# Kernel optimization log

Hardware: AMD Instinct MI355X
Metric: run time of the kernel (lower is better)

The kernel has to match this reference:

```python
import jax, jax.numpy as jnp
import numpy as np

B, S, D, H = 2, 2048, 768, 12
HD = D // H  # head dim = 64

def setup_inputs() -> dict:
    key = jax.random.key(0)
    ks = jax.random.split(key, 9)
    s = 1.0 / np.sqrt(D)
    return {
        "x": jax.random.normal(ks[0], (B, S, D), dtype=jnp.float32),
        "Wq": jax.random.uniform(ks[1], (D, D), jnp.float32, -s, s),
        "bq": jax.random.uniform(ks[2], (D,), jnp.float32, -s, s),
        "Wk": jax.random.uniform(ks[3], (D, D), jnp.float32, -s, s),
        "bk": jax.random.uniform(ks[4], (D,), jnp.float32, -s, s),
        "Wv": jax.random.uniform(ks[5], (D, D), jnp.float32, -s, s),
        "bv": jax.random.uniform(ks[6], (D,), jnp.float32, -s, s),
        "Wo": jax.random.uniform(ks[7], (D, D), jnp.float32, -s, s),
        "bo": jax.random.uniform(ks[8], (D,), jnp.float32, -s, s),
    }

def reference(x, Wq, bq, Wk, bk, Wv, bv, Wo, bo):
    b, s, _ = x.shape
    # linear projections, split into heads: [b, h, s, hd]
    def proj(W, bias):
        y = x @ W + bias
        return y.reshape(b, s, H, HD).transpose(0, 2, 1, 3)
    q = proj(Wq, bq)
    k = proj(Wk, bk)
    v = proj(Wv, bv)
    scale = 1.0 / np.sqrt(HD).astype(np.float32)
    scores = jnp.einsum('bhqd,bhkd->bhqk', q, k) * scale
    attn = jax.nn.softmax(scores, axis=-1)
    out = jnp.einsum('bhqk,bhkd->bhqd', attn, v)
    out = out.transpose(0, 2, 1, 3).reshape(b, s, D)
    return out @ Wo + bo
```

## Files before the change

### kernel.cpp

```cpp
#include <hip/hip_runtime.h>
#include <math.h>

#define NH 12
#define SEQ 2048
#define DM 768
#define HD 64
#define NB 2
#define MT (NB * SEQ)
#define QSCL 0.18033688011112042591999058512524f

typedef short bf16x8 __attribute__((ext_vector_type(8)));
typedef float f32x16 __attribute__((ext_vector_type(16)));

__device__ __forceinline__ unsigned short bf16_rne(float x) {
    unsigned u = __float_as_uint(x);
    u += 0x7fffu + ((u >> 16) & 1u);
    return (unsigned short)(u >> 16);
}
__device__ __forceinline__ float bf16_tof(short h) {
    return __uint_as_float(((unsigned)(unsigned short)h) << 16);
}

__device__ __forceinline__ void gl_lds16(const void* g, void* s) {
    __builtin_amdgcn_global_load_lds(
        (const __attribute__((address_space(1))) unsigned int*)g,
        (__attribute__((address_space(3))) unsigned int*)s, 16, 0, 0);
}

__device__ __forceinline__ f32x16 mfma32(bf16x8 a, bf16x8 b, f32x16 c) {
    return __builtin_amdgcn_mfma_f32_32x32x16_bf16(a, b, c, 0, 0, 0);
}

__device__ __forceinline__ bf16x8 gfrag(const char* base, int row, int physblk) {
    return *(const bf16x8*)(base + row * 64 + physblk * 16);
}
__device__ __forceinline__ bf16x8 afrag(const short* base, int row, int blk) {
    return *(const bf16x8*)(base + row * 64 + ((blk ^ (row & 7)) << 3));
}

__global__ __launch_bounds__(256)
void conv_all(const float* __restrict__ x,
              const float* __restrict__ Wq, const float* __restrict__ Wk,
              const float* __restrict__ Wv, const float* __restrict__ Wo,
              short* __restrict__ xg, short* __restrict__ wdst)
{
    int b = blockIdx.x;
    if (b < 1536) {
        const int idx = b * 256 + threadIdx.x;
        const int m = idx / 96, bk = idx % 96;
        const float* src = x + (size_t)m * DM + bk * 8;
        float4 v0 = *(const float4*)src;
        float4 v1 = *(const float4*)(src + 4);
        const float vv[8] = {v0.x, v0.y, v0.z, v0.w, v1.x, v1.y, v1.z, v1.w};
        union { short s[8]; int4 q; } hh;
#pragma unroll
        for (int j = 0; j < 8; j++) hh.s[j] = (short)bf16_rne(vv[j]);
        const int pb = (bk & ~3) | ((bk & 3) ^ ((m >> 1) & 3));
        *(int4*)(xg + (size_t)m * DM + pb * 8) = hh.q;
    } else {
        b -= 1536;
        const int z = b / 288;
        const float* __restrict__ W = (z == 0) ? Wq : (z == 1) ? Wk : (z == 2) ? Wv : Wo;
        const int idx = (b % 288) * 256 + threadIdx.x;
        const int n = idx % 768, bk = idx / 768;
        union { short s[8]; int4 q; } hh;
#pragma unroll
        for (int j = 0; j < 8; j++) hh.s[j] = (short)bf16_rne(W[(size_t)(bk * 8 + j) * DM + n]);
        const int pb = (bk & ~3) | ((bk & 3) ^ ((n >> 1) & 3));
        *(int4*)(wdst + (size_t)z * 589824 + (size_t)n * DM + pb * 8) = hh.q;
    }
}

template<bool SWAP>
__device__ __forceinline__ void qkv_loop(const char* pA, const char* pB,
                                         short* As, short* Bs,
                                         int w, int l, f32x16* acc)
{
    const int q32 = l & 31, half = l >> 5;
    const int sel = (q32 >> 1) & 3;
    const int arow  = 32 * (w & 1) + q32;
    const int brow0 = 64 * (w >> 1) + q32;
    char* dA = (char*)As + w * 1024 + l * 16;
    char* dB = (char*)Bs + w * 1024 + l * 16;

    for (int k0 = 0; k0 < DM; k0 += 32) {
        const size_t cb = (size_t)k0 * 2;
        __syncthreads();
        gl_lds16(pA + cb, dA);
        gl_lds16(pB + cb, dB);
        gl_lds16(pB + 64 * 1536 + cb, dB + 4096);
        __syncthreads();
#pragma unroll
        for (int s = 0; s < 2; s++) {
            const int blk = (s * 2 + half) ^ sel;
            bf16x8 a  = gfrag((char*)As, arow, blk);
            bf16x8 b0 = gfrag((char*)Bs, brow0, blk);
            bf16x8 b1 = gfrag((char*)Bs, brow0 + 32, blk);
            if (SWAP) {
                acc[0] = mfma32(b0, a, acc[0]);
                acc[1] = mfma32(b1, a, acc[1]);
            } else {
                acc[0] = mfma32(a, b0, acc[0]);
                acc[1] = mfma32(a, b1, acc[1]);
            }
        }
    }
}

__global__ __launch_bounds__(256)
void gemm_qkv(const short* __restrict__ xg, const short* __restrict__ wt,
              const float* __restrict__ bq, const float* __restrict__ bkv,
              const float* __restrict__ bv,
              short* __restrict__ qg, short* __restrict__ kg, short* __restrict__ vg)
{
    const int z = blockIdx.z;
    const short* __restrict__ Bw = wt + (size_t)z * 589824;
    const float* __restrict__ bias = (z == 0) ? bq : (z == 1) ? bkv : bv;

    __shared__ short As[2048], Bs[4096];
    const int t = threadIdx.x, w = t >> 6, l = t & 63;
    const int m0 = blockIdx.y * 64, n0 = blockIdx.x * 128;
    const int q32 = l & 31, half = l >> 5;

    const char* pA = (const char*)xg + (size_t)(m0 + (t >> 2)) * 1536 + (t & 3) * 16;
    const char* pB = (const char*)Bw + (size_t)(n0 + (t >> 2)) * 1536 + (t & 3) * 16;

    f32x16 acc[2];
#pragma unroll
    for (int i = 0; i < 2; i++)
#pragma unroll
        for (int r = 0; r < 16; r++) acc[i][r] = 0.f;

    if (z == 2) {
        qkv_loop<false>(pA, pB, As, Bs, w, l, acc);
        const int nbase = n0 + 64 * (w >> 1);
        const int h = nbase >> 6;
        const int mbase = m0 + 32 * (w & 1) + 4 * half;
        const int bb = mbase >> 11;
#pragma unroll
        for (int nt = 0; nt < 2; nt++) {
            const int hd = 32 * nt + q32;
            const float bia = bias[nbase + hd];
            short* vrow = vg + ((size_t)(bb * NH + h) * HD + hd) * SEQ;
#pragma unroll
            for (int g = 0; g < 4; g++) {
                const int ss0 = (mbase & 2047) + 8 * g;
                union { unsigned short u[4]; uint2 q; } pk;
#pragma unroll
                for (int j = 0; j < 4; j++)
                    pk.u[j] = bf16_rne(acc[nt][4 * g + j] + bia);
                const int blk = ss0 >> 3;
                const int phys = (blk & ~7) | ((blk & 7) ^ (hd & 7));
                *(uint2*)(vrow + phys * 8 + (ss0 & 7)) = pk.q;
            }
        }
    } else {
        qkv_loop<true>(pA, pB, As, Bs, w, l, acc);
        short* dst = (z == 0) ? qg : kg;
        const float scl = (z == 0) ? QSCL : 1.0f;
        const int mcol = m0 + 32 * (w & 1) + q32;
        const int bb = mcol >> 11, ss = mcol & 2047;
        const int h = (n0 + 64 * (w >> 1)) >> 6;
        short* drow = dst + ((size_t)(bb * NH + h) * SEQ + ss) * HD;
#pragma unroll
        for (int nt = 0; nt < 2; nt++)
#pragma unroll
            for (int g = 0; g < 4; g++) {
                const int hd0 = 32 * nt + 8 * g + 4 * half;
                float4 b4 = *(const float4*)&bias[(h << 6) + hd0];
                const float bb4[4] = {b4.x, b4.y, b4.z, b4.w};
                union { unsigned short u[4]; uint2 q; } pk;
#pragma unroll
                for (int j = 0; j < 4; j++)
                    pk.u[j] = bf16_rne((acc[nt][4 * g + j] + bb4[j]) * scl);
                const int phys = (hd0 >> 3) ^ (ss & 7);
                *(uint2*)(drow + phys * 8 + (hd0 & 7)) = pk.q;
            }
    }
}

__global__ __launch_bounds__(256)
void attn_mfma(const short* __restrict__ qg, const short* __restrict__ kg,
               const short* __restrict__ vg,
               short* __restrict__ opart, float* __restrict__ lpart)
{
    __shared__ short Qs[8192];
    __shared__ short Ks[4096];
    __shared__ short Vt[4096];
    __shared__ short Ps[8192];

    const int t = threadIdx.x, w = t >> 6, l = t & 63;
    const int bh = blockIdx.y, q0 = blockIdx.x * 128, ks = blockIdx.z;
    const char* qp = (const char*)(qg + (size_t)bh * SEQ * HD);
    const char* kp = (const char*)(kg + (size_t)bh * SEQ * HD);
    const char* vp = (const char*)(vg + (size_t)bh * HD * SEQ);
    const int kbase = ks * 1024;

#pragma unroll
    for (int i = 0; i < 4; i++)
        gl_lds16(qp + (size_t)(q0 + w * 32 + i * 8) * 128 + l * 16,
                 (char*)Qs + (w * 32 + i * 8) * 128);
#pragma unroll
    for (int i = 0; i < 2; i++) {
        gl_lds16(kp + (size_t)(kbase + w * 16 + i * 8) * 128 + l * 16,
                 (char*)Ks + (w * 16 + i * 8) * 128);
        gl_lds16(vp + (size_t)(w * 16 + i * 8 + (l >> 3)) * 4096 + kbase * 2 + (l & 7) * 16,
                 (char*)Vt + (w * 16 + i * 8) * 128);
    }
    __syncthreads();

    const int half = l >> 5;
    const int q = l & 31;
    bf16x8 qf[4];
#pragma unroll
    for (int s = 0; s < 4; s++)
        qf[s] = afrag(Qs, w * 32 + q, half + s * 2);
    __syncthreads();

    f32x16 oacc[2], lacc;
#pragma unroll
    for (int nt = 0; nt < 2; nt++)
#pragma unroll
        for (int r = 0; r < 16; r++) oacc[nt][r] = 0.f;
#pragma unroll
    for (int r = 0; r < 16; r++) lacc[r] = 0.f;

    bf16x8 onesf;
#pragma unroll
    for (int j = 0; j < 8; j++) onesf[j] = (short)0x3F80;

    short* psw = Ps + w * 2048;

    for (int kti = 0; kti < 16; kti++) {
        const int cur = kti & 1;
        if (kti < 15) {
            const int kb0 = kbase + (kti + 1) * 64;
            char* kd = cur ? (char*)Ks : (char*)Qs;
            char* vd = cur ? (char*)Vt : (char*)(Qs + 4096);
#pragma unroll
            for (int i = 0; i < 2; i++) {
                gl_lds16(kp + (size_t)(kb0 + w * 16 + i * 8) * 128 + l * 16,
                         kd + (w * 16 + i * 8) * 128);
                gl_lds16(vp + (size_t)(w * 16 + i * 8 + (l >> 3)) * 4096 + kb0 * 2 + (l & 7) * 16,
                         vd + (w * 16 + i * 8) * 128);
            }
        }
        const short* kc = cur ? Qs : Ks;
        const short* vc = cur ? Qs + 4096 : Vt;

        f32x16 sacc[2];
#pragma unroll
        for (int nt = 0; nt < 2; nt++)
#pragma unroll
            for (int r = 0; r < 16; r++) sacc[nt][r] = 0.f;
#pragma unroll
        for (int s = 0; s < 4; s++)
#pragma unroll
            for (int nt = 0; nt < 2; nt++) {
                bf16x8 kf = afrag(kc, nt * 32 + q, half + s * 2);
                sacc[nt] = mfma32(kf, qf[s], sacc[nt]);
            }

#pragma unroll
        for (int nt = 0; nt < 2; nt++)
#pragma unroll
            for (int g = 0; g < 4; g++) {
                const float p0 = exp2f(sacc[nt][4 * g + 0]);
                const float p1 = exp2f(sacc[nt][4 * g + 1]);
                const float p2 = exp2f(sacc[nt][4 * g + 2]);
                const float p3 = exp2f(sacc[nt][4 * g + 3]);
                uint2 pk;
                pk.x = __builtin_amdgcn_perm(__float_as_uint(p1), __float_as_uint(p0), 0x07060302u);
                pk.y = __builtin_amdgcn_perm(__float_as_uint(p3), __float_as_uint(p2), 0x07060302u);
                *(uint2*)(psw + q * 64 + (((4 * nt + g) ^ (q & 7)) << 3) + 4 * half) = pk;
            }

#pragma unroll
        for (int s = 0; s < 4; s++) {
            bf16x8 pf = afrag(psw, q, half + s * 2);
            lacc = mfma32(pf, onesf, lacc);
#pragma unroll
            for (int nt = 0; nt < 2; nt++) {
                bf16x8 vf = afrag(vc, nt * 32 + q, half + s * 2);
                oacc[nt] = mfma32(pf, vf, oacc[nt]);
            }
        }
        __syncthreads();
    }

    const size_t base = (size_t)(ks * 24 + bh) * SEQ;
#pragma unroll
    for (int r = 0; r < 16; r++) {
        const int row = q0 + w * 32 + (r & 3) + 8 * (r >> 2) + 4 * half;
#pragma unroll
        for (int nt = 0; nt < 2; nt++)
            opart[(base + row) * 64 + nt * 32 + q] = (short)bf16_rne(oacc[nt][r]);
        if (q == 0) lpart[base + row] = lacc[r];
    }
}

__global__ __launch_bounds__(256)
void attn_reduce(const short* __restrict__ opart, const float* __restrict__ lpart,
                 short* __restrict__ ag)
{
    const int idx = blockIdx.x * 256 + threadIdx.x;
    const int cg = idx & 7, row = idx >> 3;
    const int bh = row >> 11, s = row & 2047;
    union { short s[8]; int4 q; } a, b, o;
    a.q = *(const int4*)(opart + ((size_t)bh * SEQ + s) * 64 + cg * 8);
    b.q = *(const int4*)(opart + ((size_t)(24 + bh) * SEQ + s) * 64 + cg * 8);
    const float inv = 1.0f / (lpart[(size_t)bh * SEQ + s] + lpart[(size_t)(24 + bh) * SEQ + s]);
#pragma unroll
    for (int j = 0; j < 8; j++)
        o.s[j] = (short)bf16_rne((bf16_tof(a.s[j]) + bf16_tof(b.s[j])) * inv);
    const int bb = bh / NH, h = bh % NH;
    const int m = bb * SEQ + s;
    const int blk = h * 8 + cg;
    const int phys = (blk & ~3) | ((blk & 3) ^ ((m >> 1) & 3));
    *(int4*)(ag + (size_t)m * DM + phys * 8) = o.q;
}

__global__ __launch_bounds__(256)
void gemm_out(const short* __restrict__ ag, const short* __restrict__ wt3,
              const float* __restrict__ bias, float* __restrict__ out)
{
    __shared__ short As[2048], Bs[2048];
    const int t = threadIdx.x, w = t >> 6, l = t & 63;
    const int m0 = blockIdx.y * 64, n0 = blockIdx.x * 64;
    const int q32 = l & 31, half = l >> 5;
    const int sel = (q32 >> 1) & 3;

    const char* pA = (const char*)ag  + (size_t)(m0 + (t >> 2)) * 1536 + (t & 3) * 16;
    const char* pB = (const char*)wt3 + (size_t)(n0 + (t >> 2)) * 1536 + (t & 3) * 16;
    char* dA = (char*)As + w * 1024 + l * 16;
    char* dB = (char*)Bs + w * 1024 + l * 16;

    const int arow = 32 * (w & 1) + q32;
    const int brow = 32 * (w >> 1) + q32;

    f32x16 acc;
#pragma unroll
    for (int r = 0; r < 16; r++) acc[r] = 0.f;

    for (int k0 = 0; k0 < DM; k0 += 32) {
        const size_t cb = (size_t)k0 * 2;
        __syncthreads();
        gl_lds16(pA + cb, dA);
        gl_lds16(pB + cb, dB);
        __syncthreads();
#pragma unroll
        for (int s = 0; s < 2; s++) {
            const int blk = (s * 2 + half) ^ sel;
            bf16x8 a = gfrag((char*)As, arow, blk);
            bf16x8 b = gfrag((char*)Bs, brow, blk);
            acc = mfma32(b, a, acc);
        }
    }

    const int mcol = m0 + 32 * (w & 1) + q32;
    const int nb0 = n0 + 32 * (w >> 1) + 4 * half;
#pragma unroll
    for (int g = 0; g < 4; g++) {
        const int ng = nb0 + 8 * g;
        float4 b4 = *(const float4*)&bias[ng];
        float4 o;
        o.x = acc[4 * g + 0] + b4.x;
        o.y = acc[4 * g + 1] + b4.y;
        o.z = acc[4 * g + 2] + b4.z;
        o.w = acc[4 * g + 3] + b4.w;
        *(float4*)&out[(size_t)mcol * DM + ng] = o;
    }
}

extern "C" void kernel_launch(void* const* d_in, const int* in_sizes, int n_in,
                              void* d_out, int out_size, void* d_ws, size_t ws_size,
                              hipStream_t stream)
{
    const float* x  = (const float*)d_in[0];
    const float* Wq = (const float*)d_in[1];
    const float* bq = (const float*)d_in[2];
    const float* Wk = (const float*)d_in[3];
    const float* bk = (const float*)d_in[4];
    const float* Wv = (const float*)d_in[5];
    const float* bv = (const float*)d_in[6];
    const float* Wo = (const float*)d_in[7];
    const float* bo = (const float*)d_in[8];
    float* out = (float*)d_out;

    const size_t BUF = (size_t)MT * DM;
    short* xg = (short*)d_ws;
    short* qg = xg + BUF;
    short* kg = qg + BUF;
    short* vg = kg + BUF;
    short* ag = vg + BUF;
    short* wt = ag + BUF;
    short* opart = wt + (size_t)4 * 589824;
    float* lpart = (float*)(opart + (size_t)2 * 24 * SEQ * HD);

    conv_all<<<2688, 256, 0, stream>>>(x, Wq, Wk, Wv, Wo, xg, wt);
    gemm_qkv<<<dim3(6, 64, 3), 256, 0, stream>>>(xg, wt, bq, bk, bv, qg, kg, vg);
    attn_mfma<<<dim3(16, 24, 2), 256, 0, stream>>>(qg, kg, vg, opart, lpart);
    attn_reduce<<<1536, 256, 0, stream>>>(opart, lpart, ag);
    gemm_out<<<dim3(12, 64), 256, 0, stream>>>(ag, wt + (size_t)3 * 589824, bo, out);
}
```

Baseline: 197.5 us.

## Double-buffer LDS with register prefetch in QKV and output GEMMs

Replaces the direct global-to-LDS loads and the two barriers per k-step with a register-staged, double-buffered pipeline. Global loads run two k-tiles ahead in registers, are written into the alternate LDS buffer while MFMAs consume the current one, and a single barrier is kept per iteration. This aims to hide global memory latency behind compute, at the cost of more LDS (double size) and more VGPRs for the staging registers, which may reduce occupancy.

Result: slower. 304.0 us (+53.9%).

```diff
diff --git a/kernel.cpp b/kernel.cpp
--- a/kernel.cpp
+++ b/kernel.cpp
@@ -73,29 +73,50 @@
 
 template<bool SWAP>
 __device__ __forceinline__ void qkv_loop(const char* pA, const char* pB,
-                                         short* As, short* Bs,
-                                         int w, int l, f32x16* acc)
-{
+                                         char* As, char* Bs,
+                                         int t, f32x16* acc)
+{
+    const int w = t >> 6, l = t & 63;
     const int q32 = l & 31, half = l >> 5;
     const int sel = (q32 >> 1) & 3;
     const int arow  = 32 * (w & 1) + q32;
     const int brow0 = 64 * (w >> 1) + q32;
-    char* dA = (char*)As + w * 1024 + l * 16;
-    char* dB = (char*)Bs + w * 1024 + l * 16;
-
-    for (int k0 = 0; k0 < DM; k0 += 32) {
-        const size_t cb = (size_t)k0 * 2;
-        __syncthreads();
-        gl_lds16(pA + cb, dA);
-        gl_lds16(pB + cb, dB);
-        gl_lds16(pB + 64 * 1536 + cb, dB + 4096);
-        __syncthreads();
+
+    uint4 ar[2], br0[2], br1[2];
+    ar[0]  = *(const uint4*)(pA);
+    br0[0] = *(const uint4*)(pB);
+    br1[0] = *(const uint4*)(pB + 64 * 1536);
+    ar[1]  = *(const uint4*)(pA + 64);
+    br0[1] = *(const uint4*)(pB + 64);
+    br1[1] = *(const uint4*)(pB + 64 * 1536 + 64);
+    *(uint4*)(As + t * 16) = ar[0];
+    *(uint4*)(Bs + t * 16) = br0[0];
+    *(uint4*)(Bs + 4096 + t * 16) = br1[0];
+    __syncthreads();
+
+    for (int ki = 0; ki < 24; ki++) {
+        const int cur = ki & 1;
+        const char* sA = As + cur * 4096;
+        const char* sB = Bs + cur * 8192;
+        if (ki < 22) {
+            const size_t cb = (size_t)(ki + 2) * 64;
+            ar[cur]  = *(const uint4*)(pA + cb);
+            br0[cur] = *(const uint4*)(pB + cb);
+            br1[cur] = *(const uint4*)(pB + 64 * 1536 + cb);
+        }
+        if (ki < 23) {
+            char* dA = As + (cur ^ 1) * 4096 + t * 16;
+            char* dB = Bs + (cur ^ 1) * 8192 + t * 16;
+            *(uint4*)dA = ar[cur ^ 1];
+            *(uint4*)dB = br0[cur ^ 1];
+            *(uint4*)(dB + 4096) = br1[cur ^ 1];
+        }
 #pragma unroll
         for (int s = 0; s < 2; s++) {
             const int blk = (s * 2 + half) ^ sel;
-            bf16x8 a  = gfrag((char*)As, arow, blk);
-            bf16x8 b0 = gfrag((char*)Bs, brow0, blk);
-            bf16x8 b1 = gfrag((char*)Bs, brow0 + 32, blk);
+            bf16x8 a  = gfrag(sA, arow, blk);
+            bf16x8 b0 = gfrag(sB, brow0, blk);
+            bf16x8 b1 = gfrag(sB, brow0 + 32, blk);
             if (SWAP) {
                 acc[0] = mfma32(b0, a, acc[0]);
                 acc[1] = mfma32(b1, a, acc[1]);
@@ -104,6 +125,7 @@
                 acc[1] = mfma32(a, b1, acc[1]);
             }
         }
+        __syncthreads();
     }
 }
 
@@ -117,7 +139,7 @@
     const short* __restrict__ Bw = wt + (size_t)z * 589824;
     const float* __restrict__ bias = (z == 0) ? bq : (z == 1) ? bkv : bv;
 
-    __shared__ short As[2048], Bs[4096];
+    __shared__ char As[8192], Bs[16384];
     const int t = threadIdx.x, w = t >> 6, l = t & 63;
     const int m0 = blockIdx.y * 64, n0 = blockIdx.x * 128;
     const int q32 = l & 31, half = l >> 5;
@@ -132,7 +154,7 @@
         for (int r = 0; r < 16; r++) acc[i][r] = 0.f;
 
     if (z == 2) {
-        qkv_loop<false>(pA, pB, As, Bs, w, l, acc);
+        qkv_loop<false>(pA, pB, As, Bs, t, acc);
         const int nbase = n0 + 64 * (w >> 1);
         const int h = nbase >> 6;
         const int mbase = m0 + 32 * (w & 1) + 4 * half;
@@ -155,7 +177,7 @@
             }
         }
     } else {
-        qkv_loop<true>(pA, pB, As, Bs, w, l, acc);
+        qkv_loop<true>(pA, pB, As, Bs, t, acc);
         short* dst = (z == 0) ? qg : kg;
         const float scl = (z == 0) ? QSCL : 1.0f;
         const int mcol = m0 + 32 * (w & 1) + q32;
@@ -324,7 +346,7 @@
 void gemm_out(const short* __restrict__ ag, const short* __restrict__ wt3,
               const float* __restrict__ bias, float* __restrict__ out)
 {
-    __shared__ short As[2048], Bs[2048];
+    __shared__ char As[8192], Bs[8192];
     const int t = threadIdx.x, w = t >> 6, l = t & 63;
     const int m0 = blockIdx.y * 64, n0 = blockIdx.x * 64;
     const int q32 = l & 31, half = l >> 5;
@@ -332,8 +354,6 @@
 
     const char* pA = (const char*)ag  + (size_t)(m0 + (t >> 2)) * 1536 + (t & 3) * 16;
     const char* pB = (const char*)wt3 + (size_t)(n0 + (t >> 2)) * 1536 + (t & 3) * 16;
-    char* dA = (char*)As + w * 1024 + l * 16;
-    char* dB = (char*)Bs + w * 1024 + l * 16;
 
     const int arow = 32 * (w & 1) + q32;
     const int brow = 32 * (w >> 1) + q32;
@@ -342,19 +362,36 @@
 #pragma unroll
     for (int r = 0; r < 16; r++) acc[r] = 0.f;
 
-    for (int k0 = 0; k0 < DM; k0 += 32) {
-        const size_t cb = (size_t)k0 * 2;
-        __syncthreads();
-        gl_lds16(pA + cb, dA);
-        gl_lds16(pB + cb, dB);
-        __syncthreads();
+    uint4 ar[2], br[2];
+    ar[0] = *(const uint4*)(pA);
+    br[0] = *(const uint4*)(pB);
+    ar[1] = *(const uint4*)(pA + 64);
+    br[1] = *(const uint4*)(pB + 64);
+    *(uint4*)(As + t * 16) = ar[0];
+    *(uint4*)(Bs + t * 16) = br[0];
+    __syncthreads();
+
+    for (int ki = 0; ki < 24; ki++) {
+        const int cur = ki & 1;
+        const char* sA = As + cur * 4096;
+        const char* sB = Bs + cur * 4096;
+        if (ki < 22) {
+            const size_t cb = (size_t)(ki + 2) * 64;
+            ar[cur] = *(const uint4*)(pA + cb);
+            br[cur] = *(const uint4*)(pB + cb);
+        }
+        if (ki < 23) {
+            *(uint4*)(As + (cur ^ 1) * 4096 + t * 16) = ar[cur ^ 1];
+            *(uint4*)(Bs + (cur ^ 1) * 4096 + t * 16) = br[cur ^ 1];
+        }
 #pragma unroll
         for (int s = 0; s < 2; s++) {
             const int blk = (s * 2 + half) ^ sel;
-            bf16x8 a = gfrag((char*)As, arow, blk);
-            bf16x8 b = gfrag((char*)Bs, brow, blk);
+            bf16x8 a = gfrag(sA, arow, blk);
+            bf16x8 b = gfrag(sB, brow, blk);
             acc = mfma32(b, a, acc);
         }
+        __syncthreads();
     }
 
     const int mcol = m0 + 32 * (w & 1) + q32;
```

## Double-buffer LDS tiles with register prefetch in QKV and output GEMMs

Applied to the files above, without the earlier changes.

Replaces the synchronous global_load_lds staging, which needed two barriers per K step, with register-prefetched global loads written into a ping-pong pair of LDS buffers. The next K slice is loaded from global memory while the current one is consumed by MFMAs, and each K step now needs one barrier. This aims to hide global load latency behind compute in both the QKV projection and the output projection. In exchange it doubles LDS usage, adds VGPRs for the prefetch registers, and routes data through registers instead of the direct-to-LDS path.

After: 195.5 us. Within noise of the previous version (-1.0%).

```diff
diff --git a/kernel.cpp b/kernel.cpp
--- a/kernel.cpp
+++ b/kernel.cpp
@@ -73,29 +73,38 @@
 
 template<bool SWAP>
 __device__ __forceinline__ void qkv_loop(const char* pA, const char* pB,
-                                         short* As, short* Bs,
-                                         int w, int l, f32x16* acc)
-{
+                                         char* As, char* Bs,
+                                         int t, f32x16* acc)
+{
+    const int w = t >> 6, l = t & 63;
     const int q32 = l & 31, half = l >> 5;
     const int sel = (q32 >> 1) & 3;
     const int arow  = 32 * (w & 1) + q32;
     const int brow0 = 64 * (w >> 1) + q32;
-    char* dA = (char*)As + w * 1024 + l * 16;
-    char* dB = (char*)Bs + w * 1024 + l * 16;
-
-    for (int k0 = 0; k0 < DM; k0 += 32) {
-        const size_t cb = (size_t)k0 * 2;
-        __syncthreads();
-        gl_lds16(pA + cb, dA);
-        gl_lds16(pB + cb, dB);
-        gl_lds16(pB + 64 * 1536 + cb, dB + 4096);
-        __syncthreads();
+    char* dA = As + t * 16;
+    char* dB = Bs + t * 16;
+
+    uint4 a0, b00, b10;
+    uint4 a1, b01, b11;
+
+    a0  = *(const uint4*)(pA);
+    b00 = *(const uint4*)(pB);
+    b10 = *(const uint4*)(pB + 64 * 1536);
+    a1  = *(const uint4*)(pA + 64);
+    b01 = *(const uint4*)(pB + 64);
+    b11 = *(const uint4*)(pB + 64 * 1536 + 64);
+    *(uint4*)dA = a0;
+    *(uint4*)dB = b00;
+    *(uint4*)(dB + 4096) = b10;
+    __syncthreads();
+
+    auto compute = [&](const char* sA, const char* sB) {
 #pragma unroll
         for (int s = 0; s < 2; s++) {
             const int blk = (s * 2 + half) ^ sel;
-            bf16x8 a  = gfrag((char*)As, arow, blk);
-            bf16x8 b0 = gfrag((char*)Bs, brow0, blk);
-            bf16x8 b1 = gfrag((char*)Bs, brow0 + 32, blk);
+            bf16x8 a  = gfrag(sA, arow, blk);
+            bf16x8 b0 = gfrag(sB, brow0, blk);
+            bf16x8 b1 = gfrag(sB, brow0 + 32, blk);
             if (SWAP) {
                 acc[0] = mfma32(b0, a, acc[0]);
                 acc[1] = mfma32(b1, a, acc[1]);
@@ -104,6 +113,34 @@
                 acc[1] = mfma32(a, b1, acc[1]);
             }
         }
+    };
+
+    for (int kb = 0; kb < 12; kb++) {
+        if (kb < 11) {
+            const size_t cb = (size_t)(2 * kb + 2) * 64;
+            a0  = *(const uint4*)(pA + cb);
+            b00 = *(const uint4*)(pB + cb);
+            b10 = *(const uint4*)(pB + 64 * 1536 + cb);
+        }
+        *(uint4*)(dA + 4096) = a1;
+        *(uint4*)(dB + 8192) = b01;
+        *(uint4*)(dB + 8192 + 4096) = b11;
+        compute(As, Bs);
+        __syncthreads();
+
+        if (kb < 11) {
+            const size_t cb = (size_t)(2 * kb + 3) * 64;
+            a1  = *(const uint4*)(pA + cb);
+            b01 = *(const uint4*)(pB + cb);
+            b11 = *(const uint4*)(pB + 64 * 1536 + cb);
+        }
+        if (kb < 11) {
+            *(uint4*)dA = a0;
+            *(uint4*)dB = b00;
+            *(uint4*)(dB + 4096) = b10;
+        }
+        compute(As + 4096, Bs + 8192);
+        __syncthreads();
     }
 }
 
@@ -117,7 +154,7 @@
     const short* __restrict__ Bw = wt + (size_t)z * 589824;
     const float* __restrict__ bias = (z == 0) ? bq : (z == 1) ? bkv : bv;
 
-    __shared__ short As[2048], Bs[4096];
+    __shared__ char As[8192], Bs[16384];
     const int t = threadIdx.x, w = t >> 6, l = t & 63;
     const int m0 = blockIdx.y * 64, n0 = blockIdx.x * 128;
     const int q32 = l & 31, half = l >> 5;
@@ -132,7 +169,7 @@
         for (int r = 0; r < 16; r++) acc[i][r] = 0.f;
 
     if (z == 2) {
-        qkv_loop<false>(pA, pB, As, Bs, w, l, acc);
+        qkv_loop<false>(pA, pB, As, Bs, t, acc);
         const int nbase = n0 + 64 * (w >> 1);
         const int h = nbase >> 6;
         const int mbase = m0 + 32 * (w & 1) + 4 * half;
@@ -155,7 +192,7 @@
             }
         }
     } else {
-        qkv_loop<true>(pA, pB, As, Bs, w, l, acc);
+        qkv_loop<true>(pA, pB, As, Bs, t, acc);
         short* dst = (z == 0) ? qg : kg;
         const float scl = (z == 0) ? QSCL : 1.0f;
         const int mcol = m0 + 32 * (w & 1) + q32;
@@ -324,7 +361,7 @@
 void gemm_out(const short* __restrict__ ag, const short* __restrict__ wt3,
               const float* __restrict__ bias, float* __restrict__ out)
 {
-    __shared__ short As[2048], Bs[2048];
+    __shared__ char As[8192], Bs[8192];
     const int t = threadIdx.x, w = t >> 6, l = t & 63;
     const int m0 = blockIdx.y * 64, n0 = blockIdx.x * 64;
     const int q32 = l & 31, half = l >> 5;
@@ -332,8 +369,8 @@
 
     const char* pA = (const char*)ag  + (size_t)(m0 + (t >> 2)) * 1536 + (t & 3) * 16;
     const char* pB = (const char*)wt3 + (size_t)(n0 + (t >> 2)) * 1536 + (t & 3) * 16;
-    char* dA = (char*)As + w * 1024 + l * 16;
-    char* dB = (char*)Bs + w * 1024 + l * 16;
+    char* dA = As + t * 16;
+    char* dB = Bs + t * 16;
 
     const int arow = 32 * (w & 1) + q32;
     const int brow = 32 * (w >> 1) + q32;
@@ -342,19 +379,45 @@
 #pragma unroll
     for (int r = 0; r < 16; r++) acc[r] = 0.f;
 
-    for (int k0 = 0; k0 < DM; k0 += 32) {
-        const size_t cb = (size_t)k0 * 2;
-        __syncthreads();
-        gl_lds16(pA + cb, dA);
-        gl_lds16(pB + cb, dB);
-        __syncthreads();
+    uint4 a0, b0, a1, b1;
+    a0 = *(const uint4*)(pA);
+    b0 = *(const uint4*)(pB);
+    a1 = *(const uint4*)(pA + 64);
+    b1 = *(const uint4*)(pB + 64);
+    *(uint4*)dA = a0;
+    *(uint4*)dB = b0;
+    __syncthreads();
+
+    for (int kb = 0; kb < 12; kb++) {
+        if (kb < 11) {
+            const size_t cb = (size_t)(2 * kb + 2) * 64;
+            a0 = *(const uint4*)(pA + cb);
+            b0 = *(const uint4*)(pB + cb);
+        }
+        *(uint4*)(dA + 4096) = a1;
+        *(uint4*)(dB + 4096) = b1;
 #pragma unroll
         for (int s = 0; s < 2; s++) {
             const int blk = (s * 2 + half) ^ sel;
-            bf16x8 a = gfrag((char*)As, arow, blk);
-            bf16x8 b = gfrag((char*)Bs, brow, blk);
-            acc = mfma32(b, a, acc);
-        }
+            acc = mfma32(gfrag(Bs, brow, blk), gfrag(As, arow, blk), acc);
+        }
+        __syncthreads();
+
+        if (kb < 11) {
+            const size_t cb = (size_t)(2 * kb + 3) * 64;
+            a1 = *(const uint4*)(pA + cb);
+            b1 = *(const uint4*)(pB + cb);
+        }
+        if (kb < 11) {
+            *(uint4*)dA = a0;
+            *(uint4*)dB = b0;
+        }
+#pragma unroll
+        for (int s = 0; s < 2; s++) {
+            const int blk = (s * 2 + half) ^ sel;
+            acc = mfma32(gfrag(Bs + 4096, brow, blk), gfrag(As + 4096, arow, blk), acc);
+        }
+        __syncthreads();
     }
 
     const int mcol = m0 + 32 * (w & 1) + q32;
```
